# Optimization experiments

Hardware: AMD Instinct MI355X
Metric: run time of the kernel (lower is better)

The kernel has to match this reference:

```python
import jax, jax.numpy as jnp
import numpy as np

N_NODES = 10000
N_EDGES = 160000
DIM = 128
NLAYERS = 3
NBASIS = 16
NSPECIES = 100
CUTOFF = 5.0


def _mlp(x, W1, b1, W2, b2):
    # FullyConnectedNet([hidden, out]) with silu on hidden, linear output
    return jax.nn.silu(x @ W1 + b1) @ W2 + b2


def setup_inputs() -> dict:
    key = jax.random.key(0)
    ks = iter(jax.random.split(key, 64))
    scale = 0.08

    def w(shape):
        return jax.random.normal(next(ks), shape, dtype=jnp.float32) * scale

    inp = {
        "species": jax.random.randint(next(ks), (N_NODES,), 0, NSPECIES, dtype=jnp.int32),
        "edge_src": jnp.sort(jax.random.randint(next(ks), (N_EDGES,), 0, N_NODES, dtype=jnp.int32)),
        "edge_dst": jax.random.randint(next(ks), (N_EDGES,), 0, N_NODES, dtype=jnp.int32),
        "distances": 0.5 + 4.4 * jax.random.uniform(next(ks), (N_EDGES,), dtype=jnp.float32),
        "vec": jax.random.normal(next(ks), (N_EDGES, 3), dtype=jnp.float32),
        "switch": jax.random.uniform(next(ks), (N_EDGES,), dtype=jnp.float32),
        "species_W": w((NSPECIES, DIM)),
        "species_b": w((DIM,)),
        "radial_W": w((NLAYERS, NBASIS, DIM)),
        "radial_b": w((NLAYERS, DIM)),
    }
    for nm, out in [("a", DIM), ("F", 1), ("f", DIM), ("R", DIM), ("r", DIM), ("u", DIM)]:
        inp[nm + "_W1"] = w((NLAYERS, DIM, DIM))
        inp[nm + "_b1"] = w((NLAYERS, DIM))
        inp[nm + "_W2"] = w((NLAYERS, DIM, out))
        inp[nm + "_b2"] = w((NLAYERS, out))
    return inp


def reference(species, edge_src, edge_dst, distances, vec, switch,
              species_W, species_b, radial_W, radial_b,
              a_W1, a_b1, a_W2, a_b2,
              F_W1, F_b1, F_W2, F_b2,
              f_W1, f_b1, f_W2, f_b2,
              R_W1, R_b1, R_W2, R_b2,
              r_W1, r_b1, r_W2, r_b2,
              u_W1, u_b1, u_W2, u_b2):
    N = species.shape[0]
    # species encoding -> species_linear Dense
    xi = jax.nn.one_hot(species, NSPECIES, dtype=jnp.float32) @ species_W + species_b  # (N, dim)
    sw = switch[:, None]                                   # (E, 1)
    dirij = vec / distances[:, None] * sw                  # (E, 3)
    # gaussian radial basis on [0, cutoff]
    centers = jnp.linspace(0.0, CUTOFF, NBASIS, dtype=jnp.float32)
    eta = jnp.float32((NBASIS / CUTOFF) ** 2)
    rb = jnp.exp(-eta * (distances[:, None] - centers) ** 2)  # (E, nbasis)

    fi = None
    di = None
    for l in range(NLAYERS):
        ai = _mlp(xi, a_W1[l], a_b1[l], a_W2[l], a_b2[l])          # (N, dim)
        Dij = rb @ radial_W[l] + radial_b[l]                        # (E, dim)
        mij = ai[edge_src] * ai[edge_dst] * Dij * sw                # (E, dim)
        xi = xi + jax.ops.segment_sum(mij, edge_src, N)
        Fij = _mlp(mij, F_W1[l], F_b1[l], F_W2[l], F_b2[l]) * dirij  # (E, 3)
        fij = _mlp(mij, f_W1[l], f_b1[l], f_W2[l], f_b2[l])[:, :, None] * Fij[:, None, :]  # (E, C, 3)
        fij_sum = jax.ops.segment_sum(fij, edge_src, N)             # (N, C, 3)
        fi = fij_sum if l == 0 else fi + fij_sum
        deltai = _mlp(xi, R_W1[l], R_b1[l], R_W2[l], R_b2[l])[:, :, None] * fi  # (N, C, 3)
        if l == 0:
            di = deltai
        else:
            phi_rij = _mlp(mij, r_W1[l], r_b1[l], r_W2[l], r_b2[l])  # (E, C)
            phi_r = jax.ops.segment_sum(phi_rij * sw, edge_src, N)   # (N, C)
            di = phi_r[:, :, None] * di + deltai
        scal = jnp.sum(fi * di, axis=-1)                             # (N, C)
        dui = -_mlp(xi, u_W1[l], u_b1[l], u_W2[l], u_b2[l]) * scal   # (N, dim) since C == dim
        xi = xi + dui
    return xi
```

## Files before the change

### kernel.cpp

```cpp
#include <hip/hip_runtime.h>
#include <hip/hip_bf16.h>

#define N_NODES 10000
#define N_EDGES 160000
#define DIM     128
#define NBASIS  16
#define LDT     136
#define NFE     (N_NODES*DIM)

typedef __bf16 bf16x8 __attribute__((ext_vector_type(8)));
typedef __bf16 bf16x4 __attribute__((ext_vector_type(4)));
typedef __bf16 bf16x2 __attribute__((ext_vector_type(2)));
typedef float  f32x4  __attribute__((ext_vector_type(4)));

__device__ __forceinline__ float silu_f(float x){
  return x * (1.0f / (1.0f + __expf(-x)));
}
__device__ __forceinline__ f32x4 mfma16(bf16x8 a, bf16x8 b, f32x4 c){
  return __builtin_amdgcn_mfma_f32_16x16x32_bf16(a,b,c,0,0,0);
}


struct WPtrs { const float* p[11]; };

template<bool WITH_R>
__global__ __launch_bounds__(256,3) void mlp_layer(
    int nodeB,
    const __bf16* __restrict__ mij,
    const int*    __restrict__ esrc, const float* __restrict__ dirv,
    const __bf16* __restrict__ fW1z, const float* __restrict__ fb1,
    const __bf16* __restrict__ fW2z, const float* __restrict__ fb2,
    const __bf16* __restrict__ FW1z, const float* __restrict__ Fb1,
    const float*  __restrict__ FW2v, const float* __restrict__ Fb2,
    const __bf16* __restrict__ rW1z, const float* __restrict__ rb1,
    const __bf16* __restrict__ rW2z, const float* __restrict__ rb2,
    const float*  __restrict__ swv,
    float* __restrict__ fiG, float* __restrict__ phiG,
    const float* __restrict__ X,
    const __bf16* __restrict__ RW1z, const float* __restrict__ Rb1,
    const __bf16* __restrict__ RW2z, const float* __restrict__ Rb2,
    const __bf16* __restrict__ uW1z, const float* __restrict__ ub1,
    const __bf16* __restrict__ uW2z, const float* __restrict__ ub2,
    float* __restrict__ Rv, float* __restrict__ uv)
{
  __shared__ __bf16 sH[128*LDT];
  __shared__ __bf16 sW[8192];
  __shared__ int    sE[128];
  __shared__ float  sDir[128*3];
  const int tid=threadIdx.x, lane=tid&63, wv=tid>>6, l15=lane&15, quad=lane>>4;

  if ((int)blockIdx.x < nodeB){
    const long row0n = (long)blockIdx.x*64 + wv*16;
    const long rA = row0n + l15;
    const bool okA = rA < N_NODES;

    bf16x8 fa[4];
    #pragma unroll
    for (int kc=0;kc<4;kc++){
      int kb=kc*32+quad*8;
      bf16x8 a;
      #pragma unroll
      for (int i=0;i<8;i++) a[i]=(__bf16)0.f;
      if (okA){
        float4 u0 = *(const float4*)(X + rA*DIM + kb);
        float4 u1 = *(const float4*)(X + rA*DIM + kb + 4);
        a[0]=(__bf16)u0.x;a[1]=(__bf16)u0.y;a[2]=(__bf16)u0.z;a[3]=(__bf16)u0.w;
        a[4]=(__bf16)u1.x;a[5]=(__bf16)u1.y;a[6]=(__bf16)u1.z;a[7]=(__bf16)u1.w;
      }
      fa[kc]=a;
    }

    f32x4 acc[8];
    auto zacc = [&](){
      #pragma unroll
      for (int ni=0;ni<8;++ni) acc[ni]=(f32x4){0.f,0.f,0.f,0.f};
    };
    auto gemmA = [&](const __bf16* __restrict__ Wz){
      #pragma unroll
      for (int kc=0;kc<4;kc++){
        #pragma unroll
        for (int ni=0;ni<8;ni++){
          bf16x8 w = *(const bf16x8*)(Wz + (long)(kc*512 + ni*64 + lane)*8);
          acc[ni]=mfma16(w,fa[kc],acc[ni]);
        }
      }
    };
    auto gemmH = [&](const __bf16* __restrict__ Wz){
      #pragma unroll
      for (int kc=0;kc<4;kc++){
        bf16x8 h0=*(bf16x8*)&sH[(wv*16+l15)*LDT + kc*32 + quad*8];
        #pragma unroll
        for (int ni=0;ni<8;ni++){
          bf16x8 w = *(const bf16x8*)(Wz + (long)(kc*512 + ni*64 + lane)*8);
          acc[ni]=mfma16(w,h0,acc[ni]);
        }
      }
    };
    auto hEpi = [&](const float* __restrict__ b1){
      #pragma unroll
      for (int ni=0;ni<8;++ni){
        int n0 = ni*16 + quad*4;
        float4 bb = *(const float4*)(b1 + n0);
        bf16x4 h;
        h[0]=(__bf16)silu_f(acc[ni][0]+bb.x);
        h[1]=(__bf16)silu_f(acc[ni][1]+bb.y);
        h[2]=(__bf16)silu_f(acc[ni][2]+bb.z);
        h[3]=(__bf16)silu_f(acc[ni][3]+bb.w);
        *(bf16x4*)&sH[(wv*16+l15)*LDT + n0] = h;
      }
    };
    auto cStoreF = [&](const float* __restrict__ b2, float* __restrict__ Y){
      if (okA){
        #pragma unroll
        for (int ni=0;ni<8;++ni){
          int n0 = ni*16 + quad*4;
          float4 bb = *(const float4*)(b2 + n0);
          float4 o;
          o.x=acc[ni][0]+bb.x; o.y=acc[ni][1]+bb.y;
          o.z=acc[ni][2]+bb.z; o.w=acc[ni][3]+bb.w;
          *(float4*)(Y + rA*DIM + n0) = o;
        }
      }
    };

    zacc(); gemmA(RW1z); hEpi(Rb1);
    zacc(); gemmH(RW2z); cStoreF(Rb2, Rv);
    zacc(); gemmA(uW1z); hEpi(ub1);
    zacc(); gemmH(uW2z); cStoreF(ub2, uv);
    return;
  }

  const long row0 = (long)(blockIdx.x - nodeB)*128;
  const int  rloc0 = wv*32 + l15;
  const long rB0 = row0 + rloc0, rB1 = rB0+16;

  if (tid < 32)  *(int4*)&sE[tid*4]    = *(const int4*)(esrc + row0 + tid*4);
  if (tid >= 64 && tid < 160)
    *(float4*)&sDir[(tid-64)*4] = *(const float4*)(dirv + row0*3 + (tid-64)*4);

  bf16x8 fb[2][4];
  #pragma unroll
  for (int kc=0;kc<4;kc++){
    fb[0][kc] = *(const bf16x8*)(mij + rB0*DIM + kc*32 + quad*8);
    fb[1][kc] = *(const bf16x8*)(mij + rB1*DIM + kc*32 + quad*8);
  }
  float swr[2];
  if constexpr (WITH_R){ swr[0]=swv[rB0]; swr[1]=swv[rB1]; }

  f32x4 acc[2][8];
  bf16x8 pre[4];
  float eF[2];

  auto preload = [&](const __bf16* __restrict__ Wz, int half){
    #pragma unroll
    for (int it=0; it<4; ++it)
      pre[it] = *(const bf16x8*)(Wz + (long)(half*1024 + it*256 + tid)*8);
  };
  auto writePre = [&](){
    #pragma unroll
    for (int it=0; it<4; ++it)
      *(bf16x8*)&sW[(it*256+tid)*8] = pre[it];
  };
  auto zacc = [&](){
    #pragma unroll
    for (int mi=0;mi<2;++mi)
      #pragma unroll
      for (int ni=0;ni<8;++ni) acc[mi][ni]=(f32x4){0.f,0.f,0.f,0.f};
  };
  auto mfmaB = [&](int half){
    #pragma unroll
    for (int k2=0;k2<2;k2++){
      int kc = half*2 + k2;
      #pragma unroll
      for (int ni=0;ni<8;ni++){
        bf16x8 w = *(bf16x8*)&sW[(k2*512 + ni*64 + lane)*8];
        acc[0][ni]=mfma16(w,fb[0][kc],acc[0][ni]);
        acc[1][ni]=mfma16(w,fb[1][kc],acc[1][ni]);
      }
    }
  };
  auto mfmaH = [&](int half){
    #pragma unroll
    for (int k2=0;k2<2;k2++){
      int kc = half*2 + k2;
      bf16x8 h0=*(bf16x8*)&sH[(rloc0   )*LDT + kc*32 + quad*8];
      bf16x8 h1=*(bf16x8*)&sH[(rloc0+16)*LDT + kc*32 + quad*8];
      #pragma unroll
      for (int ni=0;ni<8;ni++){
        bf16x8 w = *(bf16x8*)&sW[(k2*512 + ni*64 + lane)*8];
        acc[0][ni]=mfma16(w,h0,acc[0][ni]);
        acc[1][ni]=mfma16(w,h1,acc[1][ni]);
      }
    }
  };
  auto fEpi = [&](){
    float fb2v = Fb2[0];
    #pragma unroll
    for (int mi=0;mi<2;++mi){
      float p = 0.f;
      #pragma unroll
      for (int ni=0;ni<8;++ni){
        int n0 = ni*16 + quad*4;
        float4 bb = *(const float4*)(Fb1 + n0);
        float4 w2 = *(const float4*)(FW2v + n0);
        p += silu_f(acc[mi][ni][0]+bb.x)*w2.x;
        p += silu_f(acc[mi][ni][1]+bb.y)*w2.y;
        p += silu_f(acc[mi][ni][2]+bb.z)*w2.z;
        p += silu_f(acc[mi][ni][3]+bb.w)*w2.w;
      }
      p += __shfl_xor(p,16);
      p += __shfl_xor(p,32);
      eF[mi] = p + fb2v;
    }
  };
  auto hEpi = [&](const float* __restrict__ b1){
    #pragma unroll
    for (int mi=0;mi<2;++mi){
      int rl = wv*32 + mi*16 + l15;
      #pragma unroll
      for (int ni=0;ni<8;++ni){
        int n0 = ni*16 + quad*4;
        float4 bb = *(const float4*)(b1 + n0);
        bf16x4 h;
        h[0]=(__bf16)silu_f(acc[mi][ni][0]+bb.x);
        h[1]=(__bf16)silu_f(acc[mi][ni][1]+bb.y);
        h[2]=(__bf16)silu_f(acc[mi][ni][2]+bb.z);
        h[3]=(__bf16)silu_f(acc[mi][ni][3]+bb.w);
        *(bf16x4*)&sH[rl*LDT + n0] = h;
      }
    }
  };
  auto outLDS = [&](const float* __restrict__ b2, const float* mul){
    #pragma unroll
    for (int mi=0;mi<2;++mi){
      int rl = wv*32 + mi*16 + l15;
      #pragma unroll
      for (int ni=0;ni<8;++ni){
        int n0 = ni*16 + quad*4;
        float4 bb = *(const float4*)(b2 + n0);
        bf16x4 o;
        o[0]=(__bf16)((acc[mi][ni][0]+bb.x)*mul[mi]);
        o[1]=(__bf16)((acc[mi][ni][1]+bb.y)*mul[mi]);
        o[2]=(__bf16)((acc[mi][ni][2]+bb.z)*mul[mi]);
        o[3]=(__bf16)((acc[mi][ni][3]+bb.w)*mul[mi]);
        *(bf16x4*)&sH[rl*LDT + n0] = o;
      }
    }
  };
  auto reduceFi = [&](){
    const int d = lane*2;
    float a0=0.f,a1=0.f,a2=0.f,a3=0.f,a4=0.f,a5=0.f;
    int cur = sE[wv*32];
    for (int i=0;i<32;i++){
      int e = wv*32+i;
      int n = sE[e];
      if (n != cur){
        long b = (long)cur*DIM + d;
        atomicAdd(&fiG[0L*NFE + b  ], a0);
        atomicAdd(&fiG[0L*NFE + b+1], a3);
        atomicAdd(&fiG[1L*NFE + b  ], a1);
        atomicAdd(&fiG[1L*NFE + b+1], a4);
        atomicAdd(&fiG[2L*NFE + b  ], a2);
        atomicAdd(&fiG[2L*NFE + b+1], a5);
        a0=a1=a2=a3=a4=a5=0.f; cur=n;
      }
      bf16x2 v = *(bf16x2*)&sH[e*LDT + d];
      float vx=(float)v[0], vy=(float)v[1];
      float d0=sDir[e*3+0], d1=sDir[e*3+1], d2=sDir[e*3+2];
      a0+=vx*d0; a1+=vx*d1; a2+=vx*d2;
      a3+=vy*d0; a4+=vy*d1; a5+=vy*d2;
    }
    long b = (long)cur*DIM + d;
    atomicAdd(&fiG[0L*NFE + b  ], a0);
    atomicAdd(&fiG[0L*NFE + b+1], a3);
    atomicAdd(&fiG[1L*NFE + b  ], a1);
    atomicAdd(&fiG[1L*NFE + b+1], a4);
    atomicAdd(&fiG[2L*NFE + b  ], a2);
    atomicAdd(&fiG[2L*NFE + b+1], a5);
  };
  auto reducePhi = [&](){
    const int d = lane*2;
    float a0=0.f,a1=0.f;
    int cur = sE[wv*32];
    for (int i=0;i<32;i++){
      int e = wv*32+i;
      int n = sE[e];
      if (n != cur){
        atomicAdd(&phiG[(long)cur*DIM + d  ], a0);
        atomicAdd(&phiG[(long)cur*DIM + d+1], a1);
        a0=a1=0.f; cur=n;
      }
      bf16x2 v = *(bf16x2*)&sH[e*LDT + d];
      a0 += (float)v[0]; a1 += (float)v[1];
    }
    atomicAdd(&phiG[(long)cur*DIM + d  ], a0);
    atomicAdd(&phiG[(long)cur*DIM + d+1], a1);
  };

  preload(FW1z,0);
  __syncthreads(); writePre(); __syncthreads(); preload(FW1z,1);
  zacc(); mfmaB(0);
  __syncthreads(); writePre(); __syncthreads(); preload(fW1z,0);
  mfmaB(1);
  __syncthreads(); writePre(); __syncthreads(); preload(fW1z,1);
  fEpi();
  zacc(); mfmaB(0);
  __syncthreads(); writePre(); __syncthreads(); preload(fW2z,0);
  mfmaB(1);
  __syncthreads(); writePre(); __syncthreads(); preload(fW2z,1);
  hEpi(fb1);
  zacc(); mfmaH(0);
  __syncthreads(); writePre(); __syncthreads();
  if constexpr (WITH_R) preload(rW1z,0);
  mfmaH(1);
  outLDS(fb2, eF);
  __syncthreads();
  if constexpr (WITH_R) writePre();
  reduceFi();
  __syncthreads();

  if constexpr (WITH_R){
    preload(rW1z,1);
    zacc(); mfmaB(0);
    __syncthreads(); writePre(); __syncthreads(); preload(rW2z,0);
    mfmaB(1);
    __syncthreads(); writePre(); __syncthreads(); preload(rW2z,1);
    hEpi(rb1);
    zacc(); mfmaH(0);
    __syncthreads(); writePre(); __syncthreads();
    mfmaH(1);
    outLDS(rb2, swr);
    __syncthreads();
    reducePhi();
  }
}

__global__ __launch_bounds__(64,4) void mlp_a(
    const float* __restrict__ X,
    const __bf16* __restrict__ W1z, const float* __restrict__ b1,
    const __bf16* __restrict__ W2z, const float* __restrict__ b2,
    __bf16* __restrict__ Y)
{
  __shared__ __bf16 sH[16*LDT];
  const int lane=threadIdx.x, l15=lane&15, quad=lane>>4;
  const long row0=(long)blockIdx.x*16;
  const long rA=row0+l15;

  bf16x8 fa[4];
  #pragma unroll
  for (int kc=0;kc<4;kc++){
    int kb=kc*32+quad*8;
    float4 u0 = *(const float4*)(X + rA*DIM + kb);
    float4 u1 = *(const float4*)(X + rA*DIM + kb + 4);
    bf16x8 a;
    a[0]=(__bf16)u0.x;a[1]=(__bf16)u0.y;a[2]=(__bf16)u0.z;a[3]=(__bf16)u0.w;
    a[4]=(__bf16)u1.x;a[5]=(__bf16)u1.y;a[6]=(__bf16)u1.z;a[7]=(__bf16)u1.w;
    fa[kc]=a;
  }

  f32x4 acc[8];
  #pragma unroll
  for (int ni=0;ni<8;++ni) acc[ni]=(f32x4){0.f,0.f,0.f,0.f};
  #pragma unroll
  for (int kc=0;kc<4;kc++){
    #pragma unroll
    for (int ni=0;ni<8;ni++){
      bf16x8 w = *(const bf16x8*)(W1z + (long)(kc*512 + ni*64 + lane)*8);
      acc[ni]=mfma16(w,fa[kc],acc[ni]);
    }
  }
  #pragma unroll
  for (int ni=0;ni<8;++ni){
    int n0 = ni*16 + quad*4;
    float4 bb = *(const float4*)(b1 + n0);
    bf16x4 h;
    h[0]=(__bf16)silu_f(acc[ni][0]+bb.x);
    h[1]=(__bf16)silu_f(acc[ni][1]+bb.y);
    h[2]=(__bf16)silu_f(acc[ni][2]+bb.z);
    h[3]=(__bf16)silu_f(acc[ni][3]+bb.w);
    *(bf16x4*)&sH[l15*LDT + n0] = h;
  }
  #pragma unroll
  for (int ni=0;ni<8;++ni) acc[ni]=(f32x4){0.f,0.f,0.f,0.f};
  #pragma unroll
  for (int kc=0;kc<4;kc++){
    bf16x8 h0=*(bf16x8*)&sH[l15*LDT + kc*32 + quad*8];
    #pragma unroll
    for (int ni=0;ni<8;ni++){
      bf16x8 w = *(const bf16x8*)(W2z + (long)(kc*512 + ni*64 + lane)*8);
      acc[ni]=mfma16(w,h0,acc[ni]);
    }
  }
  #pragma unroll
  for (int ni=0;ni<8;++ni){
    int n0 = ni*16 + quad*4;
    float4 bb = *(const float4*)(b2 + n0);
    bf16x4 o;
    o[0]=(__bf16)(acc[ni][0]+bb.x);
    o[1]=(__bf16)(acc[ni][1]+bb.y);
    o[2]=(__bf16)(acc[ni][2]+bb.z);
    o[3]=(__bf16)(acc[ni][3]+bb.w);
    *(bf16x4*)(Y + rA*DIM + n0) = o;
  }
}

__global__ __launch_bounds__(256) void setup_all(
    WPtrs wp, __bf16* __restrict__ wt,
    const int* __restrict__ species, const float* __restrict__ spW,
    const float* __restrict__ spB, float* __restrict__ xi, float* __restrict__ fi,
    float* __restrict__ phi,
    const float* __restrict__ dist, const float* __restrict__ vec,
    const float* __restrict__ swv, float* __restrict__ dir, float* __restrict__ rb)
{
  const int b = blockIdx.x, tid = threadIdx.x;
  if (b < 33){
    int t = b/3, l = b%3;
    const float* src = wp.p[t] + (size_t)l*16384;
    __bf16* out = wt + (size_t)b*16384;
    for (int it=0; it<8; ++it){
      int fi_ = it*256 + tid;
      int kc = fi_>>9, ni = (fi_>>6)&7, lane = fi_&63;
      int n  = ni*16 + (lane&15);
      int k0 = kc*32 + (lane>>4)*8;
      bf16x8 v;
      #pragma unroll
      for (int j=0;j<8;++j) v[j] = (__bf16)src[(k0+j)*DIM + n];
      *(bf16x8*)(out + (size_t)fi_*8) = v;
    }
  } else if (b < 33 + 5000){
    int idx = (b-33)*256 + tid;
    int n = idx >> 7, d = idx & 127;
    xi[idx] = spW[species[n]*DIM + d] + spB[d];
    phi[idx] = 0.f;
    fi[idx] = 0.f;
    fi[NFE + idx] = 0.f;
    fi[2L*NFE + idx] = 0.f;
  } else {
    int e = (b-5033)*256 + tid;
    if (e < N_EDGES){
      float d = dist[e];
      float s = swv[e];
      float inv = s / d;
      dir[e*3+0] = vec[e*3+0]*inv;
      dir[e*3+1] = vec[e*3+1]*inv;
      dir[e*3+2] = vec[e*3+2]*inv;
      const float eta = (16.0f/5.0f)*(16.0f/5.0f);
      #pragma unroll
      for (int j=0;j<NBASIS;j++){
        float c = (float)j * (5.0f/15.0f);
        float t2 = d - c;
        rb[e*NBASIS + j] = __expf(-eta*t2*t2);
      }
    }
  }
}

__global__ __launch_bounds__(256) void mij_segsum(
    const __bf16* __restrict__ ai, const int* __restrict__ esrc, const int* __restrict__ edst,
    const float* __restrict__ swv, const float* __restrict__ rb,
    const float* __restrict__ radW, const float* __restrict__ radB,
    __bf16* __restrict__ mij, float* __restrict__ xi)
{
  __shared__ float sRb[64*NBASIS];
  __shared__ int   sS[64], sD[64];
  __shared__ float sSw[64];
  int tid = threadIdx.x;
  int e0 = blockIdx.x * 64;
  *(float4*)(sRb + tid*4) = *(const float4*)(rb + (long)e0*NBASIS + tid*4);
  if (tid < 64){
    sS[tid]  = esrc[e0+tid];
    sD[tid]  = edst[e0+tid];
    sSw[tid] = swv[e0+tid];
  }
  const int wv = tid>>6, lane = tid&63;
  const int d = lane*2;
  float2 rw[NBASIS];
  #pragma unroll
  for (int j=0;j<NBASIS;j++)
    rw[j] = *(const float2*)(radW + j*DIM + d);
  float2 rB = *(const float2*)(radB + d);
  __syncthreads();

  float sx=0.f, sy=0.f;
  int cur = sS[wv*16];
  #pragma unroll
  for (int i=0;i<16;i++){
    int el = wv*16 + i;
    int n = sS[el];
    if (n != cur){
      atomicAdd(&xi[(long)cur*DIM+d  ], sx);
      atomicAdd(&xi[(long)cur*DIM+d+1], sy);
      sx=0.f; sy=0.f; cur=n;
    }
    bf16x2 as = *(const bf16x2*)(ai + (long)n*DIM + d);
    bf16x2 ad = *(const bf16x2*)(ai + (long)sD[el]*DIM + d);
    float acc0 = 0.f, acc1 = 0.f;
    #pragma unroll
    for (int j=0;j<NBASIS;j++){
      float rbv = sRb[el*NBASIS+j];
      acc0 += rbv*rw[j].x;
      acc1 += rbv*rw[j].y;
    }
    float sw_ = sSw[el];
    float m0 = (float)as[0]*(float)ad[0]*(acc0+rB.x)*sw_;
    float m1 = (float)as[1]*(float)ad[1]*(acc1+rB.y)*sw_;
    bf16x2 m; m[0]=(__bf16)m0; m[1]=(__bf16)m1;
    *(bf16x2*)(mij + (long)(e0+el)*DIM + d) = m;
    sx += m0; sy += m1;
  }
  atomicAdd(&xi[(long)cur*DIM+d  ], sx);
  atomicAdd(&xi[(long)cur*DIM+d+1], sy);
}

__global__ __launch_bounds__(256) void node_update(
    const float* __restrict__ Rv, const float* __restrict__ uv,
    float* __restrict__ fi, float* __restrict__ di, float* __restrict__ xi,
    float* __restrict__ phi, float* __restrict__ out, int layer)
{
  long idx = (long)blockIdx.x*256 + threadIdx.x;
  float f0 = fi[idx];
  float f1 = fi[NFE + idx];
  float f2 = fi[2L*NFE + idx];
  float phi_v = (layer > 0) ? phi[idx] : 0.f;
  float Rv_ = Rv[idx];
  float fv[3] = {f0,f1,f2};
  float sc = 0.f;
  #pragma unroll
  for (int k=0;k<3;k++){
    float delta = Rv_*fv[k];
    float dv = (layer==0) ? delta : phi_v*di[(long)k*NFE + idx] + delta;
    di[(long)k*NFE + idx] = dv;
    sc += fv[k]*dv;
  }
  float nx = xi[idx] - uv[idx]*sc;
  xi[idx] = nx;
  phi[idx] = 0.f;
  if (layer == 2) out[idx] = nx;
}

extern "C" void kernel_launch(void* const* d_in, const int* in_sizes, int n_in,
                              void* d_out, int out_size, void* d_ws, size_t ws_size,
                              hipStream_t stream) {
  const int*   species = (const int*)  d_in[0];
  const int*   esrc    = (const int*)  d_in[1];
  const int*   edst    = (const int*)  d_in[2];
  const float* dist    = (const float*)d_in[3];
  const float* vec     = (const float*)d_in[4];
  const float* swv     = (const float*)d_in[5];
  const float* spW     = (const float*)d_in[6];
  const float* spB     = (const float*)d_in[7];
  const float* radW    = (const float*)d_in[8];
  const float* radB    = (const float*)d_in[9];
  const float* aW1=(const float*)d_in[10], *aB1=(const float*)d_in[11], *aW2=(const float*)d_in[12], *aB2=(const float*)d_in[13];
  const float* FW1=(const float*)d_in[14], *FB1=(const float*)d_in[15], *FW2=(const float*)d_in[16], *FB2=(const float*)d_in[17];
  const float* fW1=(const float*)d_in[18], *fB1=(const float*)d_in[19], *fW2=(const float*)d_in[20], *fB2=(const float*)d_in[21];
  const float* RW1=(const float*)d_in[22], *RB1=(const float*)d_in[23], *RW2=(const float*)d_in[24], *RB2=(const float*)d_in[25];
  const float* rW1=(const float*)d_in[26], *rB1=(const float*)d_in[27], *rW2=(const float*)d_in[28], *rB2=(const float*)d_in[29];
  const float* uW1=(const float*)d_in[30], *uB1=(const float*)d_in[31], *uW2=(const float*)d_in[32], *uB2=(const float*)d_in[33];

  const long NF = (long)N_NODES*DIM;
  const long EF = (long)N_EDGES*DIM;
  float* ws   = (float*)d_ws;
  float* xi   = ws;
  float* Rv   = xi   + NF;
  float* uv   = Rv   + NF;
  float* phi  = uv   + NF;
  float* fi   = phi  + NF;
  float* di   = fi   + 3*NF;
  float* dir  = di   + 3*NF;
  float* rb   = dir  + 3L*N_EDGES;
  char* bp = (char*)(rb + 16L*N_EDGES);
  size_t off = ((size_t)(bp - (char*)d_ws) + 15) & ~(size_t)15;
  __bf16* ai   = (__bf16*)((char*)d_ws + off);
  __bf16* mij  = ai  + NF;
  __bf16* wt   = mij + EF;

  WPtrs wp;
  wp.p[0]=aW1; wp.p[1]=aW2; wp.p[2]=FW1; wp.p[3]=fW1; wp.p[4]=fW2;
  wp.p[5]=RW1; wp.p[6]=RW2; wp.p[7]=rW1; wp.p[8]=rW2; wp.p[9]=uW1; wp.p[10]=uW2;

  setup_all<<<5658, 256, 0, stream>>>(wp, wt,
                                      species, spW, spB, xi, fi, phi,
                                      dist, vec, swv, dir, rb);

  const int nodeB = (N_NODES + 63)/64;
  const int edgeB = N_EDGES/128;
  #define WT(t,l) (wt + (size_t)((t)*3+(l))*16384)

  for (int l=0;l<3;l++){
    const long bo = (long)l*DIM;

    mlp_a<<<N_NODES/16, 64, 0, stream>>>(xi, WT(0,l), aB1+bo, WT(1,l), aB2+bo, ai);
    mij_segsum<<<N_EDGES/64, 256, 0, stream>>>(ai, esrc, edst, swv, rb,
                                               radW + (long)l*NBASIS*DIM, radB + bo,
                                               mij, xi);
    if (l == 0)
      mlp_layer<false><<<nodeB+edgeB, 256, 0, stream>>>(
          nodeB, mij, esrc, dir,
          WT(3,l), fB1+bo, WT(4,l), fB2+bo,
          WT(2,l), FB1+bo, FW2+(long)l*DIM, FB2+l,
          nullptr, nullptr, nullptr, nullptr, nullptr,
          fi, phi,
          xi, WT(5,l), RB1+bo, WT(6,l), RB2+bo,
          WT(9,l), uB1+bo, WT(10,l), uB2+bo, Rv, uv);
    else
      mlp_layer<true><<<nodeB+edgeB, 256, 0, stream>>>(
          nodeB, mij, esrc, dir,
          WT(3,l), fB1+bo, WT(4,l), fB2+bo,
          WT(2,l), FB1+bo, FW2+(long)l*DIM, FB2+l,
          WT(7,l), rB1+bo, WT(8,l), rB2+bo, swv,
          fi, phi,
          xi, WT(5,l), RB1+bo, WT(6,l), RB2+bo,
          WT(9,l), uB1+bo, WT(10,l), uB2+bo, Rv, uv);
    node_update<<<5000, 256, 0, stream>>>(Rv, uv, fi, di, xi, phi,
                                          (float*)d_out, l);
  }
}
```

Measured before the change: 512.1 us.

## Double-buffer LDS weight tiles in fused edge MLP kernel to cut barriers

Result: no change. 505.3 us, median of 2 (-1.3%).

```diff
diff --git a/kernel.cpp b/kernel.cpp
--- a/kernel.cpp
+++ b/kernel.cpp
@@ -24,7 +24,7 @@
 struct WPtrs { const float* p[11]; };
 
 template<bool WITH_R>
-__global__ __launch_bounds__(256,3) void mlp_layer(
+__global__ __launch_bounds__(256,2) void mlp_layer(
     int nodeB,
     const __bf16* __restrict__ mij,
     const int*    __restrict__ esrc, const float* __restrict__ dirv,
@@ -44,7 +44,7 @@
     float* __restrict__ Rv, float* __restrict__ uv)
 {
   __shared__ __bf16 sH[128*LDT];
-  __shared__ __bf16 sW[8192];
+  __shared__ __bf16 sW[2][8192];
   __shared__ int    sE[128];
   __shared__ float  sDir[128*3];
   const int tid=threadIdx.x, lane=tid&63, wv=tid>>6, l15=lane&15, quad=lane>>4;
@@ -156,10 +156,10 @@
     for (int it=0; it<4; ++it)
       pre[it] = *(const bf16x8*)(Wz + (long)(half*1024 + it*256 + tid)*8);
   };
-  auto writePre = [&](){
+  auto writePre = [&](int b){
     #pragma unroll
     for (int it=0; it<4; ++it)
-      *(bf16x8*)&sW[(it*256+tid)*8] = pre[it];
+      *(bf16x8*)&sW[b][(it*256+tid)*8] = pre[it];
   };
   auto zacc = [&](){
     #pragma unroll
@@ -167,19 +167,19 @@
       #pragma unroll
       for (int ni=0;ni<8;++ni) acc[mi][ni]=(f32x4){0.f,0.f,0.f,0.f};
   };
-  auto mfmaB = [&](int half){
+  auto mfmaB = [&](int b, int half){
     #pragma unroll
     for (int k2=0;k2<2;k2++){
       int kc = half*2 + k2;
       #pragma unroll
       for (int ni=0;ni<8;ni++){
-        bf16x8 w = *(bf16x8*)&sW[(k2*512 + ni*64 + lane)*8];
+        bf16x8 w = *(bf16x8*)&sW[b][(k2*512 + ni*64 + lane)*8];
         acc[0][ni]=mfma16(w,fb[0][kc],acc[0][ni]);
         acc[1][ni]=mfma16(w,fb[1][kc],acc[1][ni]);
       }
     }
   };
-  auto mfmaH = [&](int half){
+  auto mfmaH = [&](int b, int half){
     #pragma unroll
     for (int k2=0;k2<2;k2++){
       int kc = half*2 + k2;
@@ -187,7 +187,7 @@
       bf16x8 h1=*(bf16x8*)&sH[(rloc0+16)*LDT + kc*32 + quad*8];
       #pragma unroll
       for (int ni=0;ni<8;ni++){
-        bf16x8 w = *(bf16x8*)&sW[(k2*512 + ni*64 + lane)*8];
+        bf16x8 w = *(bf16x8*)&sW[b][(k2*512 + ni*64 + lane)*8];
         acc[0][ni]=mfma16(w,h0,acc[0][ni]);
         acc[1][ni]=mfma16(w,h1,acc[1][ni]);
       }
@@ -297,40 +297,53 @@
     atomicAdd(&phiG[(long)cur*DIM + d+1], a1);
   };
 
-  preload(FW1z,0);
-  __syncthreads(); writePre(); __syncthreads(); preload(FW1z,1);
-  zacc(); mfmaB(0);
-  __syncthreads(); writePre(); __syncthreads(); preload(fW1z,0);
-  mfmaB(1);
-  __syncthreads(); writePre(); __syncthreads(); preload(fW1z,1);
+  preload(FW1z,0); writePre(0);
+  __syncthreads();
+  preload(FW1z,1);
+  zacc(); mfmaB(0,0);
+  writePre(1);
+  __syncthreads();
+  preload(fW1z,0);
+  mfmaB(1,1);
+  writePre(0);
+  __syncthreads();
+  preload(fW1z,1);
   fEpi();
-  zacc(); mfmaB(0);
-  __syncthreads(); writePre(); __syncthreads(); preload(fW2z,0);
-  mfmaB(1);
-  __syncthreads(); writePre(); __syncthreads(); preload(fW2z,1);
+  zacc(); mfmaB(0,0);
+  writePre(1);
+  __syncthreads();
+  preload(fW2z,0);
+  mfmaB(1,1);
+  writePre(0);
+  __syncthreads();
+  preload(fW2z,1);
   hEpi(fb1);
-  zacc(); mfmaH(0);
-  __syncthreads(); writePre(); __syncthreads();
+  zacc(); mfmaH(0,0);
+  writePre(1);
+  __syncthreads();
   if constexpr (WITH_R) preload(rW1z,0);
-  mfmaH(1);
+  mfmaH(1,1);
   outLDS(fb2, eF);
-  __syncthreads();
-  if constexpr (WITH_R) writePre();
   reduceFi();
-  __syncthreads();
 
   if constexpr (WITH_R){
+    writePre(0);
+    __syncthreads();
     preload(rW1z,1);
-    zacc(); mfmaB(0);
-    __syncthreads(); writePre(); __syncthreads(); preload(rW2z,0);
-    mfmaB(1);
-    __syncthreads(); writePre(); __syncthreads(); preload(rW2z,1);
+    zacc(); mfmaB(0,0);
+    writePre(1);
+    __syncthreads();
+    preload(rW2z,0);
+    mfmaB(1,1);
+    writePre(0);
+    __syncthreads();
+    preload(rW2z,1);
     hEpi(rb1);
-    zacc(); mfmaH(0);
-    __syncthreads(); writePre(); __syncthreads();
-    mfmaH(1);
+    zacc(); mfmaH(0,0);
+    writePre(1);
+    __syncthreads();
+    mfmaH(1,1);
     outLDS(rb2, swr);
-    __syncthreads();
     reducePhi();
   }
 }
```
